# Kernel tuning notes

Measured on AMD Instinct MI355X. Metric: run time of the kernel, lower is better.

## Reference

```python
import jax, jax.numpy as jnp
import numpy as np

N_HEAD = 16
NUM_EXPERTS = 8
TOP_K = 2
LN_EPS = 1e-5


def setup_inputs() -> dict:
    key = jax.random.key(0)
    B, T, D = 8, 1024, 1024
    H = 4 * D
    E = NUM_EXPERTS
    ks = jax.random.split(key, 24)
    s = 0.02
    inp = {
        "x": jax.random.normal(ks[0], (B, T, D), jnp.float32),
        "ln1_g": jnp.ones((D,), jnp.float32),
        "ln1_b": jnp.zeros((D,), jnp.float32),
        "ln2_g": jnp.ones((D,), jnp.float32),
        "ln2_b": jnp.zeros((D,), jnp.float32),
        "Wq": jax.random.normal(ks[1], (D, D), jnp.float32) * s,
        "bq": jnp.zeros((D,), jnp.float32),
        "Wk": jax.random.normal(ks[2], (D, D), jnp.float32) * s,
        "bk": jnp.zeros((D,), jnp.float32),
        "Wv": jax.random.normal(ks[3], (D, D), jnp.float32) * s,
        "bv": jnp.zeros((D,), jnp.float32),
        "Wp": jax.random.normal(ks[4], (D, D), jnp.float32) * s,
        "bp": jnp.zeros((D,), jnp.float32),
        "gate_W": jax.random.normal(ks[5], (D, E), jnp.float32) * s,
        "gate_b": jnp.zeros((E,), jnp.float32),
        "exp_W1": jax.random.normal(ks[6], (E, D, H), jnp.float32) * s,
        "exp_b1": jnp.zeros((E, H), jnp.float32),
        "exp_W2": jax.random.normal(ks[7], (E, H, D), jnp.float32) * s,
        "exp_b2": jnp.zeros((E, D), jnp.float32),
    }
    return inp


def _layernorm(x, g, b):
    mu = jnp.mean(x, axis=-1, keepdims=True)
    var = jnp.mean(jnp.square(x - mu), axis=-1, keepdims=True)
    return (x - mu) * jax.lax.rsqrt(var + LN_EPS) * g + b


def _attention(h, Wq, bq, Wk, bk, Wv, bv, Wp, bp):
    B, T, D = h.shape
    hd = D // N_HEAD
    # [B,T,D] -> [B,Hh,T,hd]
    def split(z):
        return z.reshape(B, T, N_HEAD, hd).transpose(0, 2, 1, 3)
    q = split(h @ Wq + bq)
    k = split(h @ Wk + bk)
    v = split(h @ Wv + bv)
    att = jnp.einsum('bhqd,bhkd->bhqk', q, k) / jnp.sqrt(jnp.float32(hd))
    causal = jnp.tril(jnp.ones((T, T), bool))
    att = jnp.where(causal, att, -jnp.inf)
    att = jax.nn.softmax(att, axis=-1)
    y = jnp.einsum('bhqk,bhkd->bhqd', att, v)
    y = y.transpose(0, 2, 1, 3).reshape(B, T, D)
    return y @ Wp + bp


def _token_moe(h, gate_W, gate_b, exp_W1, exp_b1, exp_W2, exp_b2):
    B, T, D = h.shape
    flat = h.reshape(-1, D)                      # [N, D]
    N = flat.shape[0]
    logits = flat @ gate_W + gate_b              # [N, E]
    top_v, top_i = jax.lax.top_k(logits, TOP_K)  # [N, k]
    w = jax.nn.softmax(top_v, axis=-1)           # [N, k]
    # scatter top-k weights into dense [N, E] combine weights
    w_full = jnp.zeros((N, NUM_EXPERTS), flat.dtype)
    w_full = w_full.at[jnp.arange(N)[:, None], top_i].add(w)
    out = jnp.zeros_like(flat)
    for e in range(NUM_EXPERTS):  # small fixed expert count
        mid = jax.nn.gelu(flat @ exp_W1[e] + exp_b1[e], approximate=False)
        y_e = mid @ exp_W2[e] + exp_b2[e]
        out = out + w_full[:, e:e + 1] * y_e
    return out.reshape(B, T, D)


def reference(x, ln1_g, ln1_b, ln2_g, ln2_b, Wq, bq, Wk, bk, Wv, bv, Wp, bp,
              gate_W, gate_b, exp_W1, exp_b1, exp_W2, exp_b2):
    x = x + _attention(_layernorm(x, ln1_g, ln1_b), Wq, bq, Wk, bk, Wv, bv, Wp, bp)
    x = x + _token_moe(_layernorm(x, ln2_g, ln2_b), gate_W, gate_b,
                       exp_W1, exp_b1, exp_W2, exp_b2)
    return x
```

## Files before the change

kernel.cpp:

```cpp
#include <hip/hip_runtime.h>
#include <hip/hip_bf16.h>

#define D_MODEL 1024
#define H_MLP   4096
#define N_TOK   8192
#define T_SEQ   1024
#define NHEADS  16
#define HEAD_D  64
#define NEXPERT 8
#define LN_EPS  1e-5f
#define MAX_TILES 136
#define MAX_ROWS  (MAX_TILES * 128)
#define MB (1024 * 1024)

using f32x4 = __attribute__((ext_vector_type(4))) float;
using bh8   = __attribute__((ext_vector_type(8))) short;
typedef _Float16 h8 __attribute__((ext_vector_type(8)));

__device__ __forceinline__ unsigned short f2b(float f) {
  unsigned u = __float_as_uint(f);
  return (unsigned short)((u + 0x7FFFu + ((u >> 16) & 1u)) >> 16);
}
__device__ __forceinline__ float b2f(unsigned short h) {
  return __uint_as_float(((unsigned)h) << 16);
}
__device__ __forceinline__ void split16(float v, unsigned short& hi, unsigned short& lo) {
  const _Float16 h = (_Float16)v;
  const _Float16 l = (_Float16)(v - (float)h);
  hi = __builtin_bit_cast(unsigned short, h);
  lo = __builtin_bit_cast(unsigned short, l);
}
__device__ __forceinline__ void gll16(const unsigned short* g, unsigned short* lds) {
  __builtin_amdgcn_global_load_lds(
      (const __attribute__((address_space(1))) unsigned int*)(const void*)g,
      (__attribute__((address_space(3))) unsigned int*)(void*)lds, 16, 0, 0);
}

__global__ __launch_bounds__(256) void ln1_kernel(
    const float* __restrict__ x, const float* __restrict__ g,
    const float* __restrict__ b, unsigned short* __restrict__ oh,
    unsigned short* __restrict__ ol) {
  const int t = blockIdx.x, tid = threadIdx.x;
  const float4 v = ((const float4*)(x + (size_t)t * D_MODEL))[tid];
  float s  = v.x + v.y + v.z + v.w;
  float sq = v.x * v.x + v.y * v.y + v.z * v.z + v.w * v.w;
  __shared__ float red[8];
  #pragma unroll
  for (int o = 32; o > 0; o >>= 1) { s += __shfl_down(s, o); sq += __shfl_down(sq, o); }
  if ((tid & 63) == 0) { red[tid >> 6] = s; red[4 + (tid >> 6)] = sq; }
  __syncthreads();
  s  = red[0] + red[1] + red[2] + red[3];
  sq = red[4] + red[5] + red[6] + red[7];
  const float mu = s * (1.0f / D_MODEL);
  const float var = sq * (1.0f / D_MODEL) - mu * mu;
  const float rs = 1.0f / sqrtf(var + LN_EPS);
  const float4 gv = ((const float4*)g)[tid];
  const float4 bv = ((const float4*)b)[tid];
  float4 o;
  o.x = (v.x - mu) * rs * gv.x + bv.x;
  o.y = (v.y - mu) * rs * gv.y + bv.y;
  o.z = (v.z - mu) * rs * gv.z + bv.z;
  o.w = (v.w - mu) * rs * gv.w + bv.w;
  ushort4 hs, ls;
  split16(o.x, hs.x, ls.x); split16(o.y, hs.y, ls.y);
  split16(o.z, hs.z, ls.z); split16(o.w, hs.w, ls.w);
  ((ushort4*)(oh + (size_t)t * D_MODEL))[tid] = hs;
  ((ushort4*)(ol + (size_t)t * D_MODEL))[tid] = ls;
}

template<int MODE>
__global__ __launch_bounds__(256) void gemm_split_kernel(
    const unsigned short* __restrict__ Ah_g, const unsigned short* __restrict__ Al_g,
    const unsigned short* __restrict__ Bh_g, const unsigned short* __restrict__ Bl_g,
    const float* __restrict__ bias, const float* __restrict__ Rres,
    unsigned short* __restrict__ Ch, unsigned short* __restrict__ Cl,
    float* __restrict__ Cf, int M, int N, int K) {
  __shared__ unsigned short LAh[128 * 32], LAl[128 * 32];
  __shared__ unsigned short LBh[128 * 32], LBl[128 * 32];
  const int tid = threadIdx.x, lane = tid & 63, w = tid >> 6;
  const int bm = blockIdx.y * 128, bn = blockIdx.x * 128;
  const int wm = (w >> 1) * 64, wn = (w & 1) * 64;
  f32x4 acc[4][4];
  #pragma unroll
  for (int i = 0; i < 4; ++i)
    #pragma unroll
    for (int j = 0; j < 4; ++j) acc[i][j] = (f32x4){0.f, 0.f, 0.f, 0.f};
  const int lrow16 = lane >> 2, kq8 = (lane & 3) << 3;
  const int r0 = w * 16 + lrow16, r1 = 64 + w * 16 + lrow16;
  const size_t a0 = (size_t)(bm + r0) * K + kq8, a1 = (size_t)(bm + r1) * K + kq8;
  const size_t b0 = (size_t)(bn + r0) * K + kq8, b1 = (size_t)(bn + r1) * K + kq8;
  const int lb0 = (w * 16) * 32, lb1 = (64 + w * 16) * 32;
  const int lrow = lane & 15, lk = (lane >> 4) << 3;
  for (int k0 = 0; k0 < K; k0 += 32) {
    gll16(Ah_g + a0 + k0, &LAh[lb0]); gll16(Ah_g + a1 + k0, &LAh[lb1]);
    gll16(Al_g + a0 + k0, &LAl[lb0]); gll16(Al_g + a1 + k0, &LAl[lb1]);
    gll16(Bh_g + b0 + k0, &LBh[lb0]); gll16(Bh_g + b1 + k0, &LBh[lb1]);
    gll16(Bl_g + b0 + k0, &LBl[lb0]); gll16(Bl_g + b1 + k0, &LBl[lb1]);
    __syncthreads();
    h8 ah[4], al[4], bh[4], bl[4];
    #pragma unroll
    for (int i = 0; i < 4; ++i) {
      ah[i] = *(const h8*)&LAh[(wm + i * 16 + lrow) * 32 + lk];
      al[i] = *(const h8*)&LAl[(wm + i * 16 + lrow) * 32 + lk];
    }
    #pragma unroll
    for (int j = 0; j < 4; ++j) {
      bh[j] = *(const h8*)&LBh[(wn + j * 16 + lrow) * 32 + lk];
      bl[j] = *(const h8*)&LBl[(wn + j * 16 + lrow) * 32 + lk];
    }
    #pragma unroll
    for (int i = 0; i < 4; ++i)
      #pragma unroll
      for (int j = 0; j < 4; ++j) {
        acc[i][j] = __builtin_amdgcn_mfma_f32_16x16x32_f16(ah[i], bh[j], acc[i][j], 0, 0, 0);
        acc[i][j] = __builtin_amdgcn_mfma_f32_16x16x32_f16(ah[i], bl[j], acc[i][j], 0, 0, 0);
        acc[i][j] = __builtin_amdgcn_mfma_f32_16x16x32_f16(al[i], bh[j], acc[i][j], 0, 0, 0);
      }
    __syncthreads();
  }
  const int lc = lane & 15, lr4 = (lane >> 4) * 4;
  #pragma unroll
  for (int i = 0; i < 4; ++i)
    #pragma unroll
    for (int j = 0; j < 4; ++j) {
      const int col = bn + wn + j * 16 + lc;
      const float bsv = bias[col];
      #pragma unroll
      for (int qq = 0; qq < 4; ++qq) {
        const size_t row = (size_t)bm + wm + i * 16 + lr4 + qq;
        const size_t idx = row * N + col;
        const float v = acc[i][j][qq] + bsv;
        if (MODE == 0) {
          unsigned short hi, lo;
          split16(v, hi, lo);
          Ch[idx] = hi; Cl[idx] = lo;
        } else {
          Cf[idx] = v + Rres[idx];
        }
      }
    }
}

__global__ __launch_bounds__(256) void gemm_qkv_kernel(
    const unsigned short* __restrict__ Ah_g, const unsigned short* __restrict__ Al_g,
    const unsigned short* __restrict__ BhQ, const unsigned short* __restrict__ BlQ,
    const unsigned short* __restrict__ BhK, const unsigned short* __restrict__ BlK,
    const unsigned short* __restrict__ BhV, const unsigned short* __restrict__ BlV,
    const float* __restrict__ bq, const float* __restrict__ bk, const float* __restrict__ bv,
    unsigned short* __restrict__ Qh, unsigned short* __restrict__ Ql,
    unsigned short* __restrict__ Kh_, unsigned short* __restrict__ Kl_,
    unsigned short* __restrict__ Vh_, unsigned short* __restrict__ Vl_,
    int M, int K) {
  __shared__ unsigned short LAh[128 * 32], LAl[128 * 32];
  __shared__ unsigned short LBh[128 * 32], LBl[128 * 32];
  const int tid = threadIdx.x, lane = tid & 63, w = tid >> 6;
  const int bm = blockIdx.y * 128;
  const int bng = blockIdx.x * 128;
  const int which = bng >> 10;
  const int bn = bng & 1023;
  const unsigned short* Bh_g = (which == 0) ? BhQ : ((which == 1) ? BhK : BhV);
  const unsigned short* Bl_g = (which == 0) ? BlQ : ((which == 1) ? BlK : BlV);
  const float* bias = (which == 0) ? bq : ((which == 1) ? bk : bv);
  unsigned short* Ch = (which == 0) ? Qh : ((which == 1) ? Kh_ : Vh_);
  unsigned short* Cl = (which == 0) ? Ql : ((which == 1) ? Kl_ : Vl_);
  const int wm = (w >> 1) * 64, wn = (w & 1) * 64;
  f32x4 acc[4][4];
  #pragma unroll
  for (int i = 0; i < 4; ++i)
    #pragma unroll
    for (int j = 0; j < 4; ++j) acc[i][j] = (f32x4){0.f, 0.f, 0.f, 0.f};
  const int lrow16 = lane >> 2, kq8 = (lane & 3) << 3;
  const int r0 = w * 16 + lrow16, r1 = 64 + w * 16 + lrow16;
  const size_t a0 = (size_t)(bm + r0) * K + kq8, a1 = (size_t)(bm + r1) * K + kq8;
  const size_t b0 = (size_t)(bn + r0) * K + kq8, b1 = (size_t)(bn + r1) * K + kq8;
  const int lb0 = (w * 16) * 32, lb1 = (64 + w * 16) * 32;
  const int lrow = lane & 15, lk = (lane >> 4) << 3;
  for (int k0 = 0; k0 < K; k0 += 32) {
    gll16(Ah_g + a0 + k0, &LAh[lb0]); gll16(Ah_g + a1 + k0, &LAh[lb1]);
    gll16(Al_g + a0 + k0, &LAl[lb0]); gll16(Al_g + a1 + k0, &LAl[lb1]);
    gll16(Bh_g + b0 + k0, &LBh[lb0]); gll16(Bh_g + b1 + k0, &LBh[lb1]);
    gll16(Bl_g + b0 + k0, &LBl[lb0]); gll16(Bl_g + b1 + k0, &LBl[lb1]);
    __syncthreads();
    h8 ah[4], al[4], bh[4], bl[4];
    #pragma unroll
    for (int i = 0; i < 4; ++i) {
      ah[i] = *(const h8*)&LAh[(wm + i * 16 + lrow) * 32 + lk];
      al[i] = *(const h8*)&LAl[(wm + i * 16 + lrow) * 32 + lk];
    }
    #pragma unroll
    for (int j = 0; j < 4; ++j) {
      bh[j] = *(const h8*)&LBh[(wn + j * 16 + lrow) * 32 + lk];
      bl[j] = *(const h8*)&LBl[(wn + j * 16 + lrow) * 32 + lk];
    }
    #pragma unroll
    for (int i = 0; i < 4; ++i)
      #pragma unroll
      for (int j = 0; j < 4; ++j) {
        acc[i][j] = __builtin_amdgcn_mfma_f32_16x16x32_f16(ah[i], bh[j], acc[i][j], 0, 0, 0);
        acc[i][j] = __builtin_amdgcn_mfma_f32_16x16x32_f16(ah[i], bl[j], acc[i][j], 0, 0, 0);
        acc[i][j] = __builtin_amdgcn_mfma_f32_16x16x32_f16(al[i], bh[j], acc[i][j], 0, 0, 0);
      }
    __syncthreads();
  }
  const int lc = lane & 15, lr4 = (lane >> 4) * 4;
  #pragma unroll
  for (int i = 0; i < 4; ++i)
    #pragma unroll
    for (int j = 0; j < 4; ++j) {
      const int col = bn + wn + j * 16 + lc;
      const float bsv = bias[col];
      #pragma unroll
      for (int qq = 0; qq < 4; ++qq) {
        const size_t row = (size_t)bm + wm + i * 16 + lr4 + qq;
        const size_t idx = row * D_MODEL + col;
        const float v = acc[i][j][qq] + bsv;
        unsigned short hi, lo;
        split16(v, hi, lo);
        Ch[idx] = hi; Cl[idx] = lo;
      }
    }
}

__global__ __launch_bounds__(256) void vtrans_kernel(
    const unsigned short* __restrict__ srch, unsigned short* __restrict__ dsth,
    const unsigned short* __restrict__ srcl, unsigned short* __restrict__ dstl) {
  __shared__ unsigned short tile[64][72];
  const int tid = threadIdx.x;
  const int t0 = blockIdx.x * 64, bh = blockIdx.y;
  const int b = bh >> 4, h = bh & 15;
  const unsigned short* src = blockIdx.z ? srcl : srch;
  unsigned short* dst = blockIdx.z ? dstl : dsth;
  #pragma unroll
  for (int it = 0; it < 2; ++it) {
    const int sg = tid + it * 256;
    const int r = sg >> 3, s = sg & 7;
    *(uint4*)&tile[r][s * 8] =
        *(const uint4*)(src + ((size_t)b * T_SEQ + t0 + r) * D_MODEL + h * HEAD_D + s * 8);
  }
  __syncthreads();
  #pragma unroll
  for (int it = 0; it < 2; ++it) {
    const int sg = tid + it * 256;
    const int d = sg >> 3, s = sg & 7;
    unsigned short v8[8] __attribute__((aligned(16)));
    #pragma unroll
    for (int j = 0; j < 8; ++j) v8[j] = tile[s * 8 + j][d];
    *(uint4*)(dst + ((size_t)bh * HEAD_D + d) * T_SEQ + t0 + s * 8) = *(const uint4*)v8;
  }
}

__global__ __launch_bounds__(512) void attn_mfma_kernel(
    const unsigned short* __restrict__ qh_g, const unsigned short* __restrict__ ql_g,
    const unsigned short* __restrict__ kh_g, const unsigned short* __restrict__ kl_g,
    const unsigned short* __restrict__ vth_g, const unsigned short* __restrict__ vtl_g,
    unsigned short* __restrict__ yh, unsigned short* __restrict__ yl) {
  __shared__ unsigned short Kh[64][72], Kl[64][72], Vh[64][72], Vl[64][72];
  __shared__ float Ps[8][16][36];
  const int tid = threadIdx.x, lane = tid & 63, w = tid >> 6;
  const int g = lane >> 4, c = lane & 15;
  const int qt = (int)gridDim.x - 1 - (int)blockIdx.x;
  const int bh = blockIdx.y, b = bh >> 4, h = bh & 15;
  const size_t qrow0 = (size_t)b * T_SEQ + qt * 128;
  h8 aqh[2], aql[2];
  {
    const size_t rq = (qrow0 + w * 16 + c) * D_MODEL + h * HEAD_D + g * 8;
    aqh[0] = *(const h8*)(qh_g + rq);
    aqh[1] = *(const h8*)(qh_g + rq + 32);
    aql[0] = *(const h8*)(ql_g + rq);
    aql[1] = *(const h8*)(ql_g + rq + 32);
  }
  f32x4 oacc[4];
  #pragma unroll
  for (int i = 0; i < 4; ++i) oacc[i] = (f32x4){0.f, 0.f, 0.f, 0.f};
  float m[4] = {-3e38f, -3e38f, -3e38f, -3e38f};
  float l[4] = {0.f, 0.f, 0.f, 0.f};
  const int sgr = tid >> 3, sgs = tid & 7;
  const int nkt = 2 * qt + 2;
  for (int kt = 0; kt < nkt; ++kt) {
    const int kv0 = kt * 64;
    __syncthreads();
    {
      const size_t kb = ((size_t)b * T_SEQ + kv0 + sgr) * D_MODEL + h * HEAD_D + sgs * 8;
      const size_t vb = ((size_t)bh * HEAD_D + sgr) * T_SEQ + kv0 + sgs * 8;
      *(uint4*)&Kh[sgr][sgs * 8] = *(const uint4*)(kh_g + kb);
      *(uint4*)&Kl[sgr][sgs * 8] = *(const uint4*)(kl_g + kb);
      *(uint4*)&Vh[sgr][sgs * 8] = *(const uint4*)(vth_g + vb);
      *(uint4*)&Vl[sgr][sgs * 8] = *(const uint4*)(vtl_g + vb);
    }
    __syncthreads();
    f32x4 sv[4];
    __builtin_amdgcn_s_setprio(1);
    #pragma unroll
    for (int nt = 0; nt < 4; ++nt) {
      f32x4 s = {0.f, 0.f, 0.f, 0.f};
      #pragma unroll
      for (int ks = 0; ks < 2; ++ks) {
        const h8 bkh = *(const h8*)&Kh[nt * 16 + c][ks * 32 + g * 8];
        const h8 bkl = *(const h8*)&Kl[nt * 16 + c][ks * 32 + g * 8];
        s = __builtin_amdgcn_mfma_f32_16x16x32_f16(aqh[ks], bkh, s, 0, 0, 0);
        s = __builtin_amdgcn_mfma_f32_16x16x32_f16(aqh[ks], bkl, s, 0, 0, 0);
        s = __builtin_amdgcn_mfma_f32_16x16x32_f16(aql[ks], bkh, s, 0, 0, 0);
      }
      sv[nt] = s;
    }
    __builtin_amdgcn_s_setprio(0);
    float pm[4] = {-3e38f, -3e38f, -3e38f, -3e38f};
    #pragma unroll
    for (int nt = 0; nt < 4; ++nt)
      #pragma unroll
      for (int qq = 0; qq < 4; ++qq) {
        float sval = sv[nt][qq] * 0.125f;
        const int krow = kv0 + nt * 16 + c;
        const int qrow = qt * 128 + w * 16 + g * 4 + qq;
        sval = (krow <= qrow) ? sval : -3.0e38f;
        sv[nt][qq] = sval;
        pm[qq] = fmaxf(pm[qq], sval);
      }
    #pragma unroll
    for (int o = 1; o < 16; o <<= 1)
      #pragma unroll
      for (int qq = 0; qq < 4; ++qq) pm[qq] = fmaxf(pm[qq], __shfl_xor(pm[qq], o));
    float psum[4];
    #pragma unroll
    for (int qq = 0; qq < 4; ++qq) {
      const float mnew = fmaxf(m[qq], pm[qq]);
      const float sc = expf(m[qq] - mnew);
      m[qq] = mnew;
      l[qq] *= sc;
      #pragma unroll
      for (int dt = 0; dt < 4; ++dt) oacc[dt][qq] *= sc;
      psum[qq] = 0.f;
    }
    #pragma unroll
    for (int nt = 0; nt < 4; ++nt)
      #pragma unroll
      for (int qq = 0; qq < 4; ++qq) {
        const float p = expf(sv[nt][qq] - m[qq]);
        sv[nt][qq] = p;
        psum[qq] += p;
      }
    #pragma unroll
    for (int o = 1; o < 16; o <<= 1)
      #pragma unroll
      for (int qq = 0; qq < 4; ++qq) psum[qq] += __shfl_xor(psum[qq], o);
    #pragma unroll
    for (int qq = 0; qq < 4; ++qq) l[qq] += psum[qq];
    #pragma unroll
    for (int half = 0; half < 2; ++half) {
      #pragma unroll
      for (int nt2 = 0; nt2 < 2; ++nt2)
        #pragma unroll
        for (int qq = 0; qq < 4; ++qq)
          Ps[w][g * 4 + qq][nt2 * 16 + c] = sv[half * 2 + nt2][qq];
      const float4 p0 = *(const float4*)&Ps[w][c][g * 8];
      const float4 p1 = *(const float4*)&Ps[w][c][g * 8 + 4];
      const float pv[8] = {p0.x, p0.y, p0.z, p0.w, p1.x, p1.y, p1.z, p1.w};
      h8 pah, pal;
      #pragma unroll
      for (int j = 0; j < 8; ++j) {
        const _Float16 hi = (_Float16)pv[j];
        pah[j] = hi;
        pal[j] = (_Float16)(pv[j] - (float)hi);
      }
      __builtin_amdgcn_s_setprio(1);
      #pragma unroll
      for (int dt = 0; dt < 4; ++dt) {
        const h8 bvh = *(const h8*)&Vh[dt * 16 + c][half * 32 + g * 8];
        const h8 bvl = *(const h8*)&Vl[dt * 16 + c][half * 32 + g * 8];
        oacc[dt] = __builtin_amdgcn_mfma_f32_16x16x32_f16(pah, bvh, oacc[dt], 0, 0, 0);
        oacc[dt] = __builtin_amdgcn_mfma_f32_16x16x32_f16(pah, bvl, oacc[dt], 0, 0, 0);
        oacc[dt] = __builtin_amdgcn_mfma_f32_16x16x32_f16(pal, bvh, oacc[dt], 0, 0, 0);
      }
      __builtin_amdgcn_s_setprio(0);
      if (half == 0) __builtin_amdgcn_sched_barrier(0);
    }
  }
  #pragma unroll
  for (int qq = 0; qq < 4; ++qq) {
    const float inv = 1.0f / l[qq];
    const size_t row = (qrow0 + w * 16 + g * 4 + qq) * D_MODEL + h * HEAD_D;
    #pragma unroll
    for (int dt = 0; dt < 4; ++dt) {
      unsigned short hi, lo;
      split16(oacc[dt][qq] * inv, hi, lo);
      yh[row + dt * 16 + c] = hi;
      yl[row + dt * 16 + c] = lo;
    }
  }
}

__global__ __launch_bounds__(256) void ln2_route_kernel(
    const float* __restrict__ x1, const float* __restrict__ g,
    const float* __restrict__ b, const float* __restrict__ gW,
    const float* __restrict__ gb, unsigned short* __restrict__ h2b,
    int2* __restrict__ tok_e, float2* __restrict__ tok_w, int* __restrict__ counts) {
  const int t = blockIdx.x, tid = threadIdx.x;
  const float4 v = ((const float4*)(x1 + (size_t)t * D_MODEL))[tid];
  float s  = v.x + v.y + v.z + v.w;
  float sq = v.x * v.x + v.y * v.y + v.z * v.z + v.w * v.w;
  __shared__ float red[8];
  __shared__ float lred[4][8];
  #pragma unroll
  for (int o = 32; o > 0; o >>= 1) { s += __shfl_down(s, o); sq += __shfl_down(sq, o); }
  if ((tid & 63) == 0) { red[tid >> 6] = s; red[4 + (tid >> 6)] = sq; }
  __syncthreads();
  s  = red[0] + red[1] + red[2] + red[3];
  sq = red[4] + red[5] + red[6] + red[7];
  const float mu = s * (1.0f / D_MODEL);
  const float var = sq * (1.0f / D_MODEL) - mu * mu;
  const float rs = 1.0f / sqrtf(var + LN_EPS);
  const float4 gv = ((const float4*)g)[tid];
  const float4 bv = ((const float4*)b)[tid];
  float4 hv;
  hv.x = (v.x - mu) * rs * gv.x + bv.x;
  hv.y = (v.y - mu) * rs * gv.y + bv.y;
  hv.z = (v.z - mu) * rs * gv.z + bv.z;
  hv.w = (v.w - mu) * rs * gv.w + bv.w;
  ushort4 hs;
  hs.x = f2b(hv.x); hs.y = f2b(hv.y); hs.z = f2b(hv.z); hs.w = f2b(hv.w);
  ((ushort4*)(h2b + (size_t)t * D_MODEL))[tid] = hs;
  float lg[8];
  const float* gwr = gW + (size_t)tid * 32;
  #pragma unroll
  for (int e = 0; e < 8; ++e)
    lg[e] = hv.x * gwr[e] + hv.y * gwr[8 + e] +
            hv.z * gwr[16 + e] + hv.w * gwr[24 + e];
  #pragma unroll
  for (int o = 32; o > 0; o >>= 1)
    #pragma unroll
    for (int e = 0; e < 8; ++e) lg[e] += __shfl_down(lg[e], o);
  if ((tid & 63) == 0)
    #pragma unroll
    for (int e = 0; e < 8; ++e) lred[tid >> 6][e] = lg[e];
  __syncthreads();
  if (tid == 0) {
    float L[8];
    #pragma unroll
    for (int e = 0; e < 8; ++e)
      L[e] = lred[0][e] + lred[1][e] + lred[2][e] + lred[3][e] + gb[e];
    int e0 = 0; float v0 = L[0];
    for (int e = 1; e < 8; ++e) if (L[e] > v0) { v0 = L[e]; e0 = e; }
    int e1 = (e0 == 0) ? 1 : 0; float v1 = L[e1];
    for (int e = 0; e < 8; ++e) if (e != e0 && L[e] > v1) { v1 = L[e]; e1 = e; }
    const float ew = expf(v1 - v0);
    const float inv = 1.0f / (1.0f + ew);
    tok_e[t] = make_int2(e0, e1);
    tok_w[t] = make_float2(inv, ew * inv);
    atomicAdd(&counts[e0], 1);
    atomicAdd(&counts[e1], 1);
  }
}

__global__ void route_offsets_kernel(const int* __restrict__ counts, int* __restrict__ off_al,
    int* __restrict__ ntiles, int* __restrict__ map_e, int* __restrict__ map_row) {
  if (threadIdx.x != 0 || blockIdx.x != 0) return;
  int off = 0, ti = 0;
  for (int e = 0; e < NEXPERT; ++e) {
    off_al[e] = off;
    const int tiles = (counts[e] + 127) >> 7;
    for (int j = 0; j < tiles; ++j) { map_e[ti] = e; map_row[ti] = off + (j << 7); ++ti; }
    off += tiles << 7;
  }
  off_al[NEXPERT] = off;
  ntiles[0] = ti;
}

__global__ __launch_bounds__(256) void place_kernel(
    const int2* __restrict__ tok_e, const int* __restrict__ off_al,
    int* __restrict__ cursors, int* __restrict__ list, int2* __restrict__ tok_pos) {
  const int t = blockIdx.x * 256 + threadIdx.x;
  if (t >= N_TOK) return;
  const int2 te = tok_e[t];
  const int p0 = off_al[te.x] + atomicAdd(&cursors[te.x], 1);
  const int p1 = off_al[te.y] + atomicAdd(&cursors[te.y], 1);
  list[p0] = t; list[p1] = t;
  tok_pos[t] = make_int2(p0, p1);
}

__global__ __launch_bounds__(256) void fill_pad_kernel(
    const int* __restrict__ counts, const int* __restrict__ off_al, int* __restrict__ list) {
  const int i = blockIdx.x * 256 + threadIdx.x;
  const int e = i >> 7, j = i & 127;
  if (e >= NEXPERT) return;
  const int start = off_al[e] + counts[e];
  if (start + j < off_al[e + 1]) list[start + j] = 0;
}

__global__ void transpose_cvt_kernel(
    const float* __restrict__ in, unsigned short* __restrict__ outp, int R, int C) {
  __shared__ float tile[32][33];
  const int e = blockIdx.z;
  const float* I = in + (size_t)e * R * C;
  unsigned short* O = outp + (size_t)e * R * C;
  const int c0 = blockIdx.x * 32, r0 = blockIdx.y * 32;
  const int tx = threadIdx.x, ty = threadIdx.y;
  #pragma unroll
  for (int j = 0; j < 32; j += 8)
    tile[ty + j][tx] = I[(size_t)(r0 + ty + j) * C + c0 + tx];
  __syncthreads();
  #pragma unroll
  for (int j = 0; j < 32; j += 8)
    O[(size_t)(c0 + ty + j) * R + r0 + tx] = f2b(tile[tx][ty + j]);
}

__global__ void transpose_cvt_f16_kernel(
    const float* __restrict__ in, unsigned short* __restrict__ oh,
    unsigned short* __restrict__ ol, int R, int C) {
  __shared__ float tile[32][33];
  const int c0 = blockIdx.x * 32, r0 = blockIdx.y * 32;
  const int tx = threadIdx.x, ty = threadIdx.y;
  #pragma unroll
  for (int j = 0; j < 32; j += 8)
    tile[ty + j][tx] = in[(size_t)(r0 + ty + j) * C + c0 + tx];
  __syncthreads();
  #pragma unroll
  for (int j = 0; j < 32; j += 8) {
    unsigned short hi, lo;
    split16(tile[tx][ty + j], hi, lo);
    oh[(size_t)(c0 + ty + j) * R + r0 + tx] = hi;
    ol[(size_t)(c0 + ty + j) * R + r0 + tx] = lo;
  }
}

template<int GELU_OUT, int GATHER>
__global__ __launch_bounds__(256) void moe_gemm_kernel(
    const unsigned short* __restrict__ Abase, const unsigned short* __restrict__ Bbase,
    const float* __restrict__ biasBase, unsigned short* __restrict__ midOut,
    float* __restrict__ fOut, const int* __restrict__ list,
    const int* __restrict__ map_e, const int* __restrict__ map_row,
    const int* __restrict__ ntiles_p, int K, int N) {
  const int mt = blockIdx.y;
  if (mt >= ntiles_p[0]) return;
  const int e = map_e[mt];
  const int row0 = map_row[mt];
  const int bn = blockIdx.x * 128;
  const unsigned short* Bp = Bbase + (size_t)e * (size_t)N * (size_t)K;
  const float* bias = biasBase + (size_t)e * N;
  __shared__ unsigned short As[2 * 128 * 32];
  __shared__ unsigned short Bs[2 * 128 * 32];
  const int tid = threadIdx.x, lane = tid & 63, wid = tid >> 6;
  const int wm = (wid >> 1) * 64, wn = (wid & 1) * 64;
  f32x4 acc[4][4];
  #pragma unroll
  for (int i = 0; i < 4; ++i)
    #pragma unroll
    for (int j = 0; j < 4; ++j) acc[i][j] = (f32x4){0.f, 0.f, 0.f, 0.f};
  const int lrow16 = lane >> 2, kq8 = (lane & 3) << 3;
  const int r0 = wid * 16 + lrow16, r1 = 64 + wid * 16 + lrow16;
  size_t arow0, arow1;
  if (GATHER) {
    arow0 = (size_t)list[row0 + r0] * (size_t)K + kq8;
    arow1 = (size_t)list[row0 + r1] * (size_t)K + kq8;
  } else {
    arow0 = (size_t)(row0 + r0) * (size_t)K + kq8;
    arow1 = (size_t)(row0 + r1) * (size_t)K + kq8;
  }
  const size_t brow0 = (size_t)(bn + r0) * (size_t)K + kq8;
  const size_t brow1 = (size_t)(bn + r1) * (size_t)K + kq8;
  const int lb0 = (wid * 16) * 32, lb1 = (64 + wid * 16) * 32;
  const int lrow = lane & 15, lk = (lane >> 4) << 3;
  for (int k0 = 0; k0 < K; k0 += 64) {
    gll16(Abase + arow0 + k0, &As[lb0]);
    gll16(Abase + arow1 + k0, &As[lb1]);
    gll16(Bp + brow0 + k0, &Bs[lb0]);
    gll16(Bp + brow1 + k0, &Bs[lb1]);
    gll16(Abase + arow0 + k0 + 32, &As[4096 + lb0]);
    gll16(Abase + arow1 + k0 + 32, &As[4096 + lb1]);
    gll16(Bp + brow0 + k0 + 32, &Bs[4096 + lb0]);
    gll16(Bp + brow1 + k0 + 32, &Bs[4096 + lb1]);
    __syncthreads();
    #pragma unroll
    for (int half = 0; half < 2; ++half) {
      const int boff = half << 12;
      bh8 a[4], b[4];
      #pragma unroll
      for (int i = 0; i < 4; ++i) a[i] = *(const bh8*)&As[boff + (wm + i * 16 + lrow) * 32 + lk];
      #pragma unroll
      for (int j = 0; j < 4; ++j) b[j] = *(const bh8*)&Bs[boff + (wn + j * 16 + lrow) * 32 + lk];
      __builtin_amdgcn_s_setprio(1);
      #pragma unroll
      for (int i = 0; i < 4; ++i)
        #pragma unroll
        for (int j = 0; j < 4; ++j)
          acc[i][j] = __builtin_amdgcn_mfma_f32_16x16x32_bf16(a[i], b[j], acc[i][j], 0, 0, 0);
      __builtin_amdgcn_s_setprio(0);
    }
    __syncthreads();
  }
  const int lc = lane & 15, lr4 = (lane >> 4) * 4;
  #pragma unroll
  for (int i = 0; i < 4; ++i)
    #pragma unroll
    for (int j = 0; j < 4; ++j) {
      const int col = bn + wn + j * 16 + lc;
      const float bsv = bias[col];
      #pragma unroll
      for (int qq = 0; qq < 4; ++qq) {
        const int rowl = wm + i * 16 + lr4 + qq;
        const size_t idx = (size_t)(row0 + rowl) * N + col;
        const float xv = acc[i][j][qq] + bsv;
        if (GELU_OUT) {
          const float gel = 0.5f * xv * (1.0f + erff(xv * 0.70710678118654752f));
          midOut[idx] = f2b(gel);
        } else {
          fOut[idx] = xv;
        }
      }
    }
}

__global__ __launch_bounds__(256) void combine_kernel(
    const float* __restrict__ x1, const float* __restrict__ ylist,
    const int2* __restrict__ tok_pos, const float2* __restrict__ tok_w,
    float* __restrict__ outp) {
  const int t = blockIdx.x, tid = threadIdx.x;
  const int2 p = tok_pos[t];
  const float2 w = tok_w[t];
  const float4 a  = ((const float4*)(x1 + (size_t)t * D_MODEL))[tid];
  const float4 y0 = ((const float4*)(ylist + (size_t)p.x * D_MODEL))[tid];
  const float4 y1 = ((const float4*)(ylist + (size_t)p.y * D_MODEL))[tid];
  float4 o;
  o.x = a.x + w.x * y0.x + w.y * y1.x;
  o.y = a.y + w.x * y0.y + w.y * y1.y;
  o.z = a.z + w.x * y0.z + w.y * y1.z;
  o.w = a.w + w.x * y0.w + w.y * y1.w;
  ((float4*)(outp + (size_t)t * D_MODEL))[tid] = o;
}

extern "C" void kernel_launch(void* const* d_in, const int* in_sizes, int n_in,
                              void* d_out, int out_size, void* d_ws, size_t ws_size,
                              hipStream_t stream) {
  const float* x    = (const float*)d_in[0];
  const float* ln1g = (const float*)d_in[1];
  const float* ln1b = (const float*)d_in[2];
  const float* ln2g = (const float*)d_in[3];
  const float* ln2b = (const float*)d_in[4];
  const float* Wq   = (const float*)d_in[5];
  const float* bq   = (const float*)d_in[6];
  const float* Wk   = (const float*)d_in[7];
  const float* bk   = (const float*)d_in[8];
  const float* Wv   = (const float*)d_in[9];
  const float* bv   = (const float*)d_in[10];
  const float* Wp   = (const float*)d_in[11];
  const float* bp   = (const float*)d_in[12];
  const float* gW   = (const float*)d_in[13];
  const float* gb   = (const float*)d_in[14];
  const float* eW1  = (const float*)d_in[15];
  const float* eb1  = (const float*)d_in[16];
  const float* eW2  = (const float*)d_in[17];
  const float* eb2  = (const float*)d_in[18];
  float* out = (float*)d_out;
  (void)in_sizes; (void)n_in; (void)out_size;

  char* wsb = (char*)d_ws;
  size_t off = 0;
  auto alloc = [&](size_t bytes) -> void* {
    void* p = wsb + off;
    off += (bytes + 255) & ~(size_t)255;
    return p;
  };
  int*  counts  = (int*)alloc(32);
  int*  cursors = (int*)alloc(32);
  int*  off_al  = (int*)alloc(64);
  int*  ntiles  = (int*)alloc(64);
  int*  map_e   = (int*)alloc(MAX_TILES * 4);
  int*  map_row = (int*)alloc(MAX_TILES * 4);
  const size_t ctrl_bytes = off;
  int2*   tok_e   = (int2*)alloc((size_t)N_TOK * 8);
  float2* tok_w   = (float2*)alloc((size_t)N_TOK * 8);
  int2*   tok_pos = (int2*)alloc((size_t)N_TOK * 8);
  int*    list    = (int*)alloc((size_t)MAX_ROWS * 4);
  float* x1  = (float*)alloc((size_t)N_TOK * D_MODEL * 4);
  unsigned short* h2b = (unsigned short*)alloc((size_t)N_TOK * D_MODEL * 2);
  unsigned short* W1T = (unsigned short*)alloc((size_t)NEXPERT * D_MODEL * H_MLP * 2);
  unsigned short* W2T = (unsigned short*)alloc((size_t)NEXPERT * D_MODEL * H_MLP * 2);
  float* ylist = (float*)alloc((size_t)MAX_ROWS * D_MODEL * 4);
  unsigned short* WqTh = (unsigned short*)alloc((size_t)D_MODEL * D_MODEL * 2);
  unsigned short* WqTl = (unsigned short*)alloc((size_t)D_MODEL * D_MODEL * 2);
  unsigned short* WkTh = (unsigned short*)alloc((size_t)D_MODEL * D_MODEL * 2);
  unsigned short* WkTl = (unsigned short*)alloc((size_t)D_MODEL * D_MODEL * 2);
  unsigned short* WvTh = (unsigned short*)alloc((size_t)D_MODEL * D_MODEL * 2);
  unsigned short* WvTl = (unsigned short*)alloc((size_t)D_MODEL * D_MODEL * 2);
  unsigned short* WpTh = (unsigned short*)alloc((size_t)D_MODEL * D_MODEL * 2);
  unsigned short* WpTl = (unsigned short*)alloc((size_t)D_MODEL * D_MODEL * 2);
  char* arena = (char*)alloc((size_t)160 * MB);
  unsigned short* h1h = (unsigned short*)(arena);
  unsigned short* h1l = (unsigned short*)(arena + (size_t) 16 * MB);
  unsigned short* qh_ = (unsigned short*)(arena + (size_t) 32 * MB);
  unsigned short* ql_ = (unsigned short*)(arena + (size_t) 48 * MB);
  unsigned short* kh_ = (unsigned short*)(arena + (size_t) 64 * MB);
  unsigned short* kl_ = (unsigned short*)(arena + (size_t) 80 * MB);
  unsigned short* vh_ = (unsigned short*)(arena + (size_t) 96 * MB);
  unsigned short* vl_ = (unsigned short*)(arena + (size_t)112 * MB);
  unsigned short* vth_ = (unsigned short*)(arena + (size_t)128 * MB);
  unsigned short* vtl_ = (unsigned short*)(arena + (size_t)144 * MB);
  unsigned short* yh_ = vh_;
  unsigned short* yl_ = vl_;
  unsigned short* mid = (unsigned short*)(arena);
  if (off > ws_size) return;

  hipMemsetAsync(d_ws, 0, ctrl_bytes, stream);

  transpose_cvt_kernel<<<dim3(H_MLP / 32, D_MODEL / 32, NEXPERT), dim3(32, 8), 0, stream>>>(
      eW1, W1T, D_MODEL, H_MLP);
  transpose_cvt_kernel<<<dim3(D_MODEL / 32, H_MLP / 32, NEXPERT), dim3(32, 8), 0, stream>>>(
      eW2, W2T, H_MLP, D_MODEL);
  transpose_cvt_f16_kernel<<<dim3(32, 32), dim3(32, 8), 0, stream>>>(Wq, WqTh, WqTl, D_MODEL, D_MODEL);
  transpose_cvt_f16_kernel<<<dim3(32, 32), dim3(32, 8), 0, stream>>>(Wk, WkTh, WkTl, D_MODEL, D_MODEL);
  transpose_cvt_f16_kernel<<<dim3(32, 32), dim3(32, 8), 0, stream>>>(Wv, WvTh, WvTl, D_MODEL, D_MODEL);
  transpose_cvt_f16_kernel<<<dim3(32, 32), dim3(32, 8), 0, stream>>>(Wp, WpTh, WpTl, D_MODEL, D_MODEL);

  ln1_kernel<<<N_TOK, 256, 0, stream>>>(x, ln1g, ln1b, h1h, h1l);

  gemm_qkv_kernel<<<dim3(24, 64), 256, 0, stream>>>(
      h1h, h1l, WqTh, WqTl, WkTh, WkTl, WvTh, WvTl, bq, bk, bv,
      qh_, ql_, kh_, kl_, vh_, vl_, N_TOK, D_MODEL);

  vtrans_kernel<<<dim3(T_SEQ / 64, (N_TOK / T_SEQ) * NHEADS, 2), 256, 0, stream>>>(
      vh_, vth_, vl_, vtl_);

  attn_mfma_kernel<<<dim3(T_SEQ / 128, (N_TOK / T_SEQ) * NHEADS), 512, 0, stream>>>(
      qh_, ql_, kh_, kl_, vth_, vtl_, yh_, yl_);

  gemm_split_kernel<1><<<dim3(8, 64), 256, 0, stream>>>(
      yh_, yl_, WpTh, WpTl, bp, x, nullptr, nullptr, x1, N_TOK, D_MODEL, D_MODEL);

  ln2_route_kernel<<<N_TOK, 256, 0, stream>>>(x1, ln2g, ln2b, gW, gb, h2b, tok_e, tok_w, counts);
  route_offsets_kernel<<<1, 64, 0, stream>>>(counts, off_al, ntiles, map_e, map_row);
  place_kernel<<<N_TOK / 256, 256, 0, stream>>>(tok_e, off_al, cursors, list, tok_pos);
  fill_pad_kernel<<<4, 256, 0, stream>>>(counts, off_al, list);

  moe_gemm_kernel<1, 1><<<dim3(H_MLP / 128, MAX_TILES), 256, 0, stream>>>(
      h2b, W1T, eb1, mid, nullptr, list, map_e, map_row, ntiles, D_MODEL, H_MLP);
  moe_gemm_kernel<0, 0><<<dim3(D_MODEL / 128, MAX_TILES), 256, 0, stream>>>(
      mid, W2T, eb2, nullptr, ylist, list, map_e, map_row, ntiles, H_MLP, D_MODEL);

  combine_kernel<<<N_TOK, 256, 0, stream>>>(x1, ylist, tok_pos, tok_w, out);
}
```

Measured before the change: 1.256 ms.

## Double-buffer LDS tiles in MoE GEMM to overlap global loads with MFMA

Shared-memory buffers in the MoE expert GEMM are doubled so the next K-tile is prefetched via direct global-to-LDS loads while the current tile feeds MFMAs. The aim is to hide global load latency that was previously exposed before each compute step. In exchange, LDS per block doubles to 64 KB, which reduces how many blocks can be resident per CU.

```diff
diff --git a/kernel.cpp b/kernel.cpp
--- a/kernel.cpp
+++ b/kernel.cpp
@@ -536,8 +536,8 @@
   const int bn = blockIdx.x * 128;
   const unsigned short* Bp = Bbase + (size_t)e * (size_t)N * (size_t)K;
   const float* bias = biasBase + (size_t)e * N;
-  __shared__ unsigned short As[2 * 128 * 32];
-  __shared__ unsigned short Bs[2 * 128 * 32];
+  __shared__ unsigned short As[2 * 8192];
+  __shared__ unsigned short Bs[2 * 8192];
   const int tid = threadIdx.x, lane = tid & 63, wid = tid >> 6;
   const int wm = (wid >> 1) * 64, wn = (wid & 1) * 64;
   f32x4 acc[4][4];
@@ -559,19 +559,27 @@
   const size_t brow1 = (size_t)(bn + r1) * (size_t)K + kq8;
   const int lb0 = (wid * 16) * 32, lb1 = (64 + wid * 16) * 32;
   const int lrow = lane & 15, lk = (lane >> 4) << 3;
-  for (int k0 = 0; k0 < K; k0 += 64) {
-    gll16(Abase + arow0 + k0, &As[lb0]);
-    gll16(Abase + arow1 + k0, &As[lb1]);
-    gll16(Bp + brow0 + k0, &Bs[lb0]);
-    gll16(Bp + brow1 + k0, &Bs[lb1]);
-    gll16(Abase + arow0 + k0 + 32, &As[4096 + lb0]);
-    gll16(Abase + arow1 + k0 + 32, &As[4096 + lb1]);
-    gll16(Bp + brow0 + k0 + 32, &Bs[4096 + lb0]);
-    gll16(Bp + brow1 + k0 + 32, &Bs[4096 + lb1]);
-    __syncthreads();
+  const int NT = K >> 6;
+  auto stage = [&](int kk, int buf) {
+    const int bo = buf << 13;
+    gll16(Abase + arow0 + kk, &As[bo + lb0]);
+    gll16(Abase + arow1 + kk, &As[bo + lb1]);
+    gll16(Bp + brow0 + kk, &Bs[bo + lb0]);
+    gll16(Bp + brow1 + kk, &Bs[bo + lb1]);
+    gll16(Abase + arow0 + kk + 32, &As[bo + 4096 + lb0]);
+    gll16(Abase + arow1 + kk + 32, &As[bo + 4096 + lb1]);
+    gll16(Bp + brow0 + kk + 32, &Bs[bo + 4096 + lb0]);
+    gll16(Bp + brow1 + kk + 32, &Bs[bo + 4096 + lb1]);
+  };
+  stage(0, 0);
+  __syncthreads();
+  for (int t = 0; t < NT; ++t) {
+    const int cur = t & 1;
+    if (t + 1 < NT) stage((t + 1) << 6, cur ^ 1);
+    const int bufoff = cur << 13;
     #pragma unroll
     for (int half = 0; half < 2; ++half) {
-      const int boff = half << 12;
+      const int boff = bufoff + (half << 12);
       bh8 a[4], b[4];
       #pragma unroll
       for (int i = 0; i < 4; ++i) a[i] = *(const bh8*)&As[boff + (wm + i * 16 + lrow) * 32 + lk];
```

After: 1.353 ms. +7.7%, slower.
